# Optimization experiments

Hardware: AMD Instinct MI355X
Metric: run time of the kernel (lower is better)

Reference implementation:

```python
import jax, jax.numpy as jnp
import numpy as np

E, T, D_IN, D_HID, D_OUT = 8, 2048, 1024, 4096, 1024
INTER = 2 * D_HID  # gated (SwiGLU) -> weight1 produces [gate, val]


def setup_inputs() -> dict:
    key = jax.random.key(0)
    k_x, k_w1, k_w2 = jax.random.split(key, 3)
    # kaiming_uniform-ish scale for weights
    x = jax.random.normal(k_x, (E, T, D_IN), dtype=jnp.float32)
    w1 = jax.random.normal(k_w1, (E, D_IN, INTER), dtype=jnp.float32) * (1.0 / np.sqrt(D_IN))
    w2 = jax.random.normal(k_w2, (E, D_HID, D_OUT), dtype=jnp.float32) * (1.0 / np.sqrt(D_HID))
    return {"x": x, "weight1": w1, "weight2": w2}


def reference(x, weight1, weight2):
    # h: [E, T, 2*D_HID] grouped GEMM over experts
    h = jnp.einsum("etd,edi->eti", x, weight1)
    gate, val = jnp.split(h, 2, axis=-1)
    h = jax.nn.silu(gate) * val  # SwiGLU; dropout is identity in eval / p=0
    out = jnp.einsum("eth,eho->eto", h, weight2)  # [E, T, D_OUT]
    return out
```

## Files before the change

### kernel.cpp

```cpp
#include <hip/hip_runtime.h>


#define E_    8
#define T_    2048
#define DIN   1024
#define DHID  4096
#define DOUT  1024
#define INTER 8192

#define NB_W1   16384
#define NB_CONV 2048
#define NB_W2   8192

typedef _Float16 f16;
typedef _Float16 f16x8 __attribute__((ext_vector_type(8)));
typedef float    f32x4 __attribute__((ext_vector_type(4)));

typedef const __attribute__((address_space(1))) void gvoid_t;
typedef __attribute__((address_space(3))) void lvoid_t;

__device__ __forceinline__ void gload_lds16(const void* g, void* l) {
  __builtin_amdgcn_global_load_lds((gvoid_t*)g, (lvoid_t*)l, 16, 0, 0);
}

__device__ __forceinline__ void conv_body(
    const float* __restrict__ src, f16* __restrict__ dst, int n8,
    int bid, int nblk) {
  int i = bid * 256 + threadIdx.x;
  int stride = nblk * 256;
  for (; i < n8; i += stride) {
    const float4* s = (const float4*)(src + (size_t)i * 8);
    float4 a0 = s[0], a1 = s[1];
    f16x8 v;
    v[0] = (f16)a0.x; v[1] = (f16)a0.y; v[2] = (f16)a0.z; v[3] = (f16)a0.w;
    v[4] = (f16)a1.x; v[5] = (f16)a1.y; v[6] = (f16)a1.z; v[7] = (f16)a1.w;
    *(f16x8*)(dst + (size_t)i * 8) = v;
  }
}

template <typename TileT>
__device__ __forceinline__ void xpose64_body(
    const float* __restrict__ src, f16* __restrict__ dst,
    int R, int C, int tC, int bid, TileT& tile) {
  int perE = (R >> 6) * tC;
  int e = bid / perE;
  int rem = bid - e * perE;
  int rt = rem / tC;
  int ct = rem - rt * tC;
  int r0 = rt << 6, c0 = ct << 6;
  int t = threadIdx.x;
  int lr  = t >> 2;
  int lc4 = (t & 3) * 16;
  const float* s = src + (size_t)e * R * C + (size_t)(r0 + lr) * C + c0 + lc4;
#pragma unroll
  for (int i = 0; i < 4; ++i) {
    float4 v = *(const float4*)(s + i * 4);
    tile[lr][lc4 + i * 4 + 0] = (f16)v.x;
    tile[lr][lc4 + i * 4 + 1] = (f16)v.y;
    tile[lr][lc4 + i * 4 + 2] = (f16)v.z;
    tile[lr][lc4 + i * 4 + 3] = (f16)v.w;
  }
  __syncthreads();
  f16* d = dst + (size_t)e * C * R + (size_t)(c0 + lr) * R + r0 + lc4;
  f16x8 o0, o1;
#pragma unroll
  for (int j = 0; j < 8; ++j) o0[j] = tile[lc4 + j][lr];
#pragma unroll
  for (int j = 0; j < 8; ++j) o1[j] = tile[lc4 + 8 + j][lr];
  *(f16x8*)(d)     = o0;
  *(f16x8*)(d + 8) = o1;
}

__global__ __launch_bounds__(256) void prep_all(
    const float* __restrict__ x,  f16* __restrict__ xh,
    const float* __restrict__ w1, f16* __restrict__ w1t,
    const float* __restrict__ w2, f16* __restrict__ w2t) {
  __shared__ f16 tile[64][72];
  int bid = blockIdx.x;
  if (bid < NB_W1) {
    xpose64_body(w1, w1t, DIN, INTER, INTER / 64, bid, tile);
  } else if (bid < NB_W1 + NB_CONV) {
    conv_body(x, xh, E_ * T_ * DIN / 8, bid - NB_W1, NB_CONV);
  } else {
    xpose64_body(w2, w2t, DHID, DOUT, DOUT / 64, bid - (NB_W1 + NB_CONV), tile);
  }
}

__global__ __launch_bounds__(256) void conv_f32_f16(
    const float* __restrict__ src, f16* __restrict__ dst, int n8) {
  conv_body(src, dst, n8, blockIdx.x, gridDim.x);
}

__global__ __launch_bounds__(256) void xpose64_f32_f16(
    const float* __restrict__ src, f16* __restrict__ dst,
    int R, int C, int tC) {
  __shared__ f16 tile[64][72];
  xpose64_body(src, dst, R, C, tC, blockIdx.x, tile);
}

__global__ __launch_bounds__(512, 2) void gemm1_swiglu_xh(
    const f16* __restrict__ xh,
    const f16* __restrict__ w1t,
    f16* __restrict__ hact) {
  __shared__ __align__(1024) f16 As[128][64];
  __shared__ __align__(1024) f16 Bg[128][64];
  __shared__ __align__(1024) f16 Bv[128][64];

  int bid = blockIdx.x;
  int e   = bid >> 9;
  int rem = bid & 511;
  int mt  = rem >> 5;
  int nt  = rem & 31;
  int m0 = mt * 128, n0 = nt * 128;

  const f16* xe = xh  + ((size_t)e * T_ + m0) * DIN;
  const f16* wg = w1t + ((size_t)e * INTER + n0) * DIN;
  const f16* wv = w1t + ((size_t)e * INTER + DHID + n0) * DIN;

  int tid  = threadIdx.x;
  int lane = tid & 63;
  int wid  = tid >> 6;

  int srow8 = lane >> 3;
  int scol  = ((lane & 7) ^ srow8) * 8;

  auto stA = [&](int kt, int i) {
    int ci = wid + 8 * i;
    gload_lds16(xe + (size_t)(ci * 8 + srow8) * DIN + kt * 64 + scol,
                (char*)&As[0][0] + ci * 1024);
  };
  auto stG = [&](int kt, int i) {
    int ci = wid + 8 * i;
    gload_lds16(wg + (size_t)(ci * 8 + srow8) * DIN + kt * 64 + scol,
                (char*)&Bg[0][0] + ci * 1024);
  };
  auto stV = [&](int kt, int i) {
    int ci = wid + 8 * i;
    gload_lds16(wv + (size_t)(ci * 8 + srow8) * DIN + kt * 64 + scol,
                (char*)&Bv[0][0] + ci * 1024);
  };

  int wm  = wid >> 2;
  int wn  = wid & 3;
  int lr  = lane & 15;
  int l16 = lane >> 4;

  f32x4 accG[4][2], accV[4][2];
#pragma unroll
  for (int m = 0; m < 4; ++m)
#pragma unroll
    for (int n = 0; n < 2; ++n) {
      accG[m][n] = f32x4{0.f, 0.f, 0.f, 0.f};
      accV[m][n] = f32x4{0.f, 0.f, 0.f, 0.f};
    }

  for (int kt = 0; kt < DIN / 64; ++kt) {
    __syncthreads();
    stA(kt, 0); stA(kt, 1);
    stG(kt, 0); stG(kt, 1);
    stV(kt, 0); stV(kt, 1);
    __syncthreads();

    f16x8 af[4][2], bg[2][2], bv[2][2];
#pragma unroll
    for (int m = 0; m < 4; ++m)
#pragma unroll
      for (int kk = 0; kk < 2; ++kk) {
        int row_ = wm * 64 + m * 16 + lr;
        af[m][kk] = *(const f16x8*)((const char*)&As[0][0] + row_ * 128 +
                                    (((kk * 4 + l16) ^ (lr & 7)) << 4));
      }
#pragma unroll
    for (int n = 0; n < 2; ++n)
#pragma unroll
      for (int kk = 0; kk < 2; ++kk) {
        int row_ = wn * 32 + n * 16 + lr;
        bg[n][kk] = *(const f16x8*)((const char*)&Bg[0][0] + row_ * 128 +
                                    (((kk * 4 + l16) ^ (lr & 7)) << 4));
        bv[n][kk] = *(const f16x8*)((const char*)&Bv[0][0] + row_ * 128 +
                                    (((kk * 4 + l16) ^ (lr & 7)) << 4));
      }
#pragma unroll
    for (int m = 0; m < 4; ++m)
#pragma unroll
      for (int n = 0; n < 2; ++n)
#pragma unroll
        for (int kk = 0; kk < 2; ++kk) {
          accG[m][n] = __builtin_amdgcn_mfma_f32_16x16x32_f16(af[m][kk], bg[n][kk], accG[m][n], 0, 0, 0);
          accV[m][n] = __builtin_amdgcn_mfma_f32_16x16x32_f16(af[m][kk], bv[n][kk], accV[m][n], 0, 0, 0);
        }
  }

  f16* he = hact + (size_t)e * T_ * DHID;
  int rbase = m0 + wm * 64 + l16 * 4;
  int cbase = n0 + wn * 32 + lr;
#pragma unroll
  for (int m = 0; m < 4; ++m)
#pragma unroll
    for (int n = 0; n < 2; ++n)
#pragma unroll
      for (int j = 0; j < 4; ++j) {
        int row = rbase + m * 16 + j;
        int col = cbase + n * 16;
        float g = accG[m][n][j];
        float v = accV[m][n][j];
        float s = g / (1.0f + __expf(-g));
        he[(size_t)row * DHID + col] = (f16)(s * v);
      }
}

__global__ __launch_bounds__(512, 2) void gemm1_swiglu_rs(
    const float* __restrict__ x,
    const f16* __restrict__ w1t,
    f16* __restrict__ hact) {
  __shared__ f16 As[128][36];
  __shared__ f16 Bg[128][32];
  __shared__ f16 Bv[128][32];

  int bid = blockIdx.x;
  int e   = bid >> 9;
  int rem = bid & 511;
  int mt  = rem >> 5;
  int nt  = rem & 31;
  int m0 = mt * 128, n0 = nt * 128;

  const float* xe = x   + ((size_t)e * T_ + m0) * DIN;
  const f16*   wg = w1t + ((size_t)e * INTER + n0) * DIN;
  const f16*   wv = w1t + ((size_t)e * INTER + DHID + n0) * DIN;

  int tid  = threadIdx.x;
  int lane = tid & 63;
  int wid  = tid >> 6;

  int arow = tid >> 2;
  int acol = (tid & 3) * 8;
  int brow = wid * 16 + (lane >> 2);
  int bcol = (lane & 3) * 8;
  f16* lG = &Bg[wid * 16][0];
  f16* lV = &Bv[wid * 16][0];

  int wm = wid >> 2;
  int wn = wid & 3;
  int lr = lane & 15;
  int lk = (lane >> 4) * 8;

  f32x4 accG[4][2], accV[4][2];
#pragma unroll
  for (int m = 0; m < 4; ++m)
#pragma unroll
    for (int n = 0; n < 2; ++n) {
      accG[m][n] = f32x4{0.f, 0.f, 0.f, 0.f};
      accV[m][n] = f32x4{0.f, 0.f, 0.f, 0.f};
    }

  for (int k = 0; k < DIN; k += 32) {
    __syncthreads();
    gload_lds16(wg + (size_t)brow * DIN + k + bcol, lG);
    gload_lds16(wv + (size_t)brow * DIN + k + bcol, lV);
    {
      const float* sa = xe + (size_t)arow * DIN + k + acol;
      float4 a0 = ((const float4*)sa)[0];
      float4 a1 = ((const float4*)sa)[1];
      f16x8 v;
      v[0] = (f16)a0.x; v[1] = (f16)a0.y; v[2] = (f16)a0.z; v[3] = (f16)a0.w;
      v[4] = (f16)a1.x; v[5] = (f16)a1.y; v[6] = (f16)a1.z; v[7] = (f16)a1.w;
      *(f16x8*)&As[arow][acol] = v;
    }
    __syncthreads();

    f16x8 af[4], bg[2], bv[2];
#pragma unroll
    for (int m = 0; m < 4; ++m)
      af[m] = *(const f16x8*)&As[wm * 64 + m * 16 + lr][lk];
#pragma unroll
    for (int n = 0; n < 2; ++n) {
      bg[n] = *(const f16x8*)&Bg[wn * 32 + n * 16 + lr][lk];
      bv[n] = *(const f16x8*)&Bv[wn * 32 + n * 16 + lr][lk];
    }
#pragma unroll
    for (int m = 0; m < 4; ++m)
#pragma unroll
      for (int n = 0; n < 2; ++n) {
        accG[m][n] = __builtin_amdgcn_mfma_f32_16x16x32_f16(af[m], bg[n], accG[m][n], 0, 0, 0);
        accV[m][n] = __builtin_amdgcn_mfma_f32_16x16x32_f16(af[m], bv[n], accV[m][n], 0, 0, 0);
      }
  }

  f16* he = hact + (size_t)e * T_ * DHID;
  int rbase = m0 + wm * 64 + (lane >> 4) * 4;
  int cbase = n0 + wn * 32 + lr;
#pragma unroll
  for (int m = 0; m < 4; ++m)
#pragma unroll
    for (int n = 0; n < 2; ++n)
#pragma unroll
      for (int j = 0; j < 4; ++j) {
        int row = rbase + m * 16 + j;
        int col = cbase + n * 16;
        float g = accG[m][n][j];
        float v = accV[m][n][j];
        float s = g / (1.0f + __expf(-g));
        he[(size_t)row * DHID + col] = (f16)(s * v);
      }
}

__global__ __launch_bounds__(512, 2) void gemm2_8ph(
    const f16* __restrict__ hact,
    const f16* __restrict__ w2t,
    float* __restrict__ out) {
  __shared__ __align__(1024) f16 As[2][256][64];
  __shared__ __align__(1024) f16 Bs[2][256][64];

  int bid = blockIdx.x;
  int e   = bid >> 5;
  int rem = bid & 31;
  int mt  = rem >> 2;
  int nt  = rem & 3;
  int m0 = mt * 256, n0 = nt * 256;

  const f16* ha = hact + ((size_t)e * T_ + m0) * DHID;
  const f16* wb = w2t  + ((size_t)e * DOUT + n0) * DHID;

  int tid  = threadIdx.x;
  int lane = tid & 63;
  int wid  = tid >> 6;
  int wm   = wid >> 2;
  int wn   = wid & 3;
  int lr   = lane & 15;
  int l16  = lane >> 4;

  int srow = lane >> 3;
  int scol = ((lane & 7) ^ srow) * 8;

  auto stA = [&](int buf, int kt, int i) {
    int ci = wid + 8 * i;
    gload_lds16(ha + (size_t)(ci * 8 + srow) * DHID + kt * 64 + scol,
                (char*)&As[buf][0][0] + ci * 1024);
  };
  auto stB = [&](int buf, int kt, int i) {
    int ci = wid + 8 * i;
    gload_lds16(wb + (size_t)(ci * 8 + srow) * DHID + kt * 64 + scol,
                (char*)&Bs[buf][0][0] + ci * 1024);
  };

  f32x4 acc[8][4];
#pragma unroll
  for (int m = 0; m < 8; ++m)
#pragma unroll
    for (int n = 0; n < 4; ++n) acc[m][n] = f32x4{0.f, 0.f, 0.f, 0.f};

  f16x8 af[4][2], bf0[2][2], bf1[2][2];

#define READ_A2(b, MH)                                                       \
  _Pragma("unroll") for (int m = 0; m < 4; ++m)                              \
  _Pragma("unroll") for (int kk = 0; kk < 2; ++kk) {                         \
    int row_ = wm * 128 + (MH) * 64 + m * 16 + lr;                           \
    af[m][kk] = *(const f16x8*)((const char*)&As[b][0][0] + row_ * 128 +     \
                                (((kk * 4 + l16) ^ (lr & 7)) << 4));         \
  }
#define READ_B2(b, NH, DST)                                                  \
  _Pragma("unroll") for (int n = 0; n < 2; ++n)                              \
  _Pragma("unroll") for (int kk = 0; kk < 2; ++kk) {                         \
    int row_ = wn * 64 + (NH) * 32 + n * 16 + lr;                            \
    DST[n][kk] = *(const f16x8*)((const char*)&Bs[b][0][0] + row_ * 128 +    \
                                 (((kk * 4 + l16) ^ (lr & 7)) << 4));        \
  }
#define MFMA16Q(MH, NH, BB)                                                  \
  __builtin_amdgcn_s_setprio(1);                                            \
  _Pragma("unroll") for (int m = 0; m < 4; ++m)                              \
  _Pragma("unroll") for (int n = 0; n < 2; ++n)                              \
  _Pragma("unroll") for (int kk = 0; kk < 2; ++kk)                          \
    acc[(MH) * 4 + m][(NH) * 2 + n] = __builtin_amdgcn_mfma_f32_16x16x32_f16(\
        af[m][kk], BB[n][kk], acc[(MH) * 4 + m][(NH) * 2 + n], 0, 0, 0);     \
  __builtin_amdgcn_s_setprio(0);
#define BAR() __builtin_amdgcn_s_barrier()
#define LGKM0() asm volatile("s_waitcnt lgkmcnt(0)" ::: "memory")
#define VM6() asm volatile("s_waitcnt vmcnt(6)" ::: "memory")

  stA(0, 0, 0); stA(0, 0, 1); stA(0, 0, 2); stA(0, 0, 3);
  stB(0, 0, 0); stB(0, 0, 1); stB(0, 0, 2); stB(0, 0, 3);
  stB(1, 1, 0); stB(1, 1, 1); stB(1, 1, 2); stB(1, 1, 3);
  stA(1, 1, 0); stA(1, 1, 1);
  VM6();
  BAR();

  for (int it = 0; it < 32; ++it) {
    int tb = 2 * it + 1;
    int pa = (2 * it + 2) & 63;
    int pb = (2 * it + 3) & 63;

    READ_A2(0, 0); READ_B2(0, 0, bf0);
    stA(1, tb, 2); stA(1, tb, 3);
    BAR(); LGKM0();
    MFMA16Q(0, 0, bf0);
    BAR();

    READ_B2(0, 1, bf1);
    BAR(); LGKM0();
    MFMA16Q(0, 1, bf1);
    BAR();

    READ_A2(0, 1);
    stB(0, pa, 0); stB(0, pa, 1);
    BAR(); LGKM0();
    MFMA16Q(1, 0, bf0);
    BAR();

    stB(0, pa, 2); stB(0, pa, 3);
    stA(0, pa, 0); stA(0, pa, 1);
    BAR();
    MFMA16Q(1, 1, bf1);
    VM6();
    BAR();

    READ_A2(1, 0); READ_B2(1, 0, bf0);
    stA(0, pa, 2); stA(0, pa, 3);
    BAR(); LGKM0();
    MFMA16Q(0, 0, bf0);
    BAR();

    READ_B2(1, 1, bf1);
    BAR(); LGKM0();
    MFMA16Q(0, 1, bf1);
    BAR();

    READ_A2(1, 1);
    stB(1, pb, 0); stB(1, pb, 1);
    BAR(); LGKM0();
    MFMA16Q(1, 0, bf0);
    BAR();

    stB(1, pb, 2); stB(1, pb, 3);
    stA(1, pb, 0); stA(1, pb, 1);
    BAR();
    MFMA16Q(1, 1, bf1);
    VM6();
    BAR();
  }

#undef READ_A2
#undef READ_B2
#undef MFMA16Q
#undef BAR
#undef LGKM0
#undef VM6

  float* oe = out + (size_t)e * T_ * DOUT;
  int rbase = m0 + wm * 128 + l16 * 4;
  int cbase = n0 + wn * 64 + lr;
#pragma unroll
  for (int m = 0; m < 8; ++m)
#pragma unroll
    for (int n = 0; n < 4; ++n)
#pragma unroll
      for (int j = 0; j < 4; ++j) {
        int row = rbase + m * 16 + j;
        int col = cbase + n * 16;
        oe[(size_t)row * DOUT + col] = acc[m][n][j];
      }
}

extern "C" void kernel_launch(void* const* d_in, const int* in_sizes, int n_in,
                              void* d_out, int out_size, void* d_ws, size_t ws_size,
                              hipStream_t stream) {
  const float* x  = (const float*)d_in[0];
  const float* w1 = (const float*)d_in[1];
  const float* w2 = (const float*)d_in[2];
  float* out = (float*)d_out;

  const size_t HACT_B = (size_t)E_ * T_ * DHID * 2;
  const size_t W1T_B  = (size_t)E_ * INTER * DIN * 2;
  const size_t W2T_B  = (size_t)E_ * DOUT * DHID * 2;
  const size_t XH_B   = (size_t)E_ * T_ * DIN * 2;

  f16* hact = (f16*)d_ws;
  f16* w1t  = (f16*)((char*)d_ws + HACT_B);

  if (ws_size >= HACT_B + W1T_B + W2T_B + XH_B) {
    f16* w2t = (f16*)((char*)d_ws + HACT_B + W1T_B);
    f16* xxh = (f16*)((char*)d_ws + HACT_B + W1T_B + W2T_B);
    prep_all<<<NB_W1 + NB_CONV + NB_W2, 256, 0, stream>>>(
        x, xxh, w1, w1t, w2, w2t);
    gemm1_swiglu_xh<<<E_ * 16 * 32, 512, 0, stream>>>(xxh, w1t, hact);
    gemm2_8ph<<<E_ * 8 * 4, 512, 0, stream>>>(hact, w2t, out);
  } else if (ws_size >= HACT_B + W1T_B + XH_B) {
    f16* xxh = (f16*)((char*)d_ws + HACT_B + W1T_B);
    xpose64_f32_f16<<<E_ * (DIN / 64) * (INTER / 64), 256, 0, stream>>>(
        w1, w1t, DIN, INTER, INTER / 64);
    conv_f32_f16<<<2048, 256, 0, stream>>>(x, xxh, E_ * T_ * DIN / 8);
    gemm1_swiglu_xh<<<E_ * 16 * 32, 512, 0, stream>>>(xxh, w1t, hact);
    xpose64_f32_f16<<<E_ * (DHID / 64) * (DOUT / 64), 256, 0, stream>>>(
        w2, w1t, DHID, DOUT, DOUT / 64);
    gemm2_8ph<<<E_ * 8 * 4, 512, 0, stream>>>(hact, w1t, out);
  } else {
    xpose64_f32_f16<<<E_ * (DIN / 64) * (INTER / 64), 256, 0, stream>>>(
        w1, w1t, DIN, INTER, INTER / 64);
    gemm1_swiglu_rs<<<E_ * 16 * 32, 512, 0, stream>>>(x, w1t, hact);
    xpose64_f32_f16<<<E_ * (DHID / 64) * (DOUT / 64), 256, 0, stream>>>(
        w2, w1t, DHID, DOUT, DOUT / 64);
    gemm2_8ph<<<E_ * 8 * 4, 512, 0, stream>>>(hact, w1t, out);
  }
}
```

Measured before the change: 567.7 us.

## Fold W2 transpose into GEMM1 launch to overlap with matmul

```diff
diff --git a/kernel.cpp b/kernel.cpp
--- a/kernel.cpp
+++ b/kernel.cpp
@@ -10,7 +10,8 @@
 
 #define NB_W1   16384
 #define NB_CONV 2048
-#define NB_W2   8192
+#define NB_G1   4096
+#define NB_X2   4096
 
 typedef _Float16 f16;
 typedef _Float16 f16x8 __attribute__((ext_vector_type(8)));
@@ -38,17 +39,15 @@
   }
 }
 
-template <typename TileT>
-__device__ __forceinline__ void xpose64_body(
+__device__ __forceinline__ void xpose64_tile(
     const float* __restrict__ src, f16* __restrict__ dst,
-    int R, int C, int tC, int bid, TileT& tile) {
+    int R, int C, int tC, int tileIdx, f16 (*tile)[72], int t) {
   int perE = (R >> 6) * tC;
-  int e = bid / perE;
-  int rem = bid - e * perE;
+  int e = tileIdx / perE;
+  int rem = tileIdx - e * perE;
   int rt = rem / tC;
   int ct = rem - rt * tC;
   int r0 = rt << 6, c0 = ct << 6;
-  int t = threadIdx.x;
   int lr  = t >> 2;
   int lc4 = (t & 3) * 16;
   const float* s = src + (size_t)e * R * C + (size_t)(r0 + lr) * C + c0 + lc4;
@@ -71,18 +70,15 @@
   *(f16x8*)(d + 8) = o1;
 }
 
-__global__ __launch_bounds__(256) void prep_all(
+__global__ __launch_bounds__(256) void prep_w1_conv(
     const float* __restrict__ x,  f16* __restrict__ xh,
-    const float* __restrict__ w1, f16* __restrict__ w1t,
-    const float* __restrict__ w2, f16* __restrict__ w2t) {
+    const float* __restrict__ w1, f16* __restrict__ w1t) {
   __shared__ f16 tile[64][72];
   int bid = blockIdx.x;
   if (bid < NB_W1) {
-    xpose64_body(w1, w1t, DIN, INTER, INTER / 64, bid, tile);
-  } else if (bid < NB_W1 + NB_CONV) {
+    xpose64_tile(w1, w1t, DIN, INTER, INTER / 64, bid, tile, threadIdx.x);
+  } else {
     conv_body(x, xh, E_ * T_ * DIN / 8, bid - NB_W1, NB_CONV);
-  } else {
-    xpose64_body(w2, w2t, DHID, DOUT, DOUT / 64, bid - (NB_W1 + NB_CONV), tile);
   }
 }
 
@@ -95,7 +91,129 @@
     const float* __restrict__ src, f16* __restrict__ dst,
     int R, int C, int tC) {
   __shared__ f16 tile[64][72];
-  xpose64_body(src, dst, R, C, tC, blockIdx.x, tile);
+  xpose64_tile(src, dst, R, C, tC, blockIdx.x, tile, threadIdx.x);
+}
+
+__global__ __launch_bounds__(512, 2) void gemm1_swiglu_w2x(
+    const f16* __restrict__ xh,
+    const f16* __restrict__ w1t,
+    f16* __restrict__ hact,
+    const float* __restrict__ w2,
+    f16* __restrict__ w2t) {
+  __shared__ __align__(1024) f16 As[128][64];
+  __shared__ __align__(1024) f16 Bg[128][64];
+  __shared__ __align__(1024) f16 Bv[128][64];
+
+  int bid = blockIdx.x;
+  if (bid >= NB_G1) {
+    int half = threadIdx.x >> 8;
+    int t    = threadIdx.x & 255;
+    int tileIdx = (bid - NB_G1) * 2 + half;
+    f16 (*tile)[72] = (f16(*)[72])((char*)&As[0][0] + half * 9216);
+    xpose64_tile(w2, w2t, DHID, DOUT, DOUT / 64, tileIdx, tile, t);
+    return;
+  }
+
+  int e   = bid >> 9;
+  int rem = bid & 511;
+  int mt  = rem >> 5;
+  int nt  = rem & 31;
+  int m0 = mt * 128, n0 = nt * 128;
+
+  const f16* xe = xh  + ((size_t)e * T_ + m0) * DIN;
+  const f16* wg = w1t + ((size_t)e * INTER + n0) * DIN;
+  const f16* wv = w1t + ((size_t)e * INTER + DHID + n0) * DIN;
+
+  int tid  = threadIdx.x;
+  int lane = tid & 63;
+  int wid  = tid >> 6;
+
+  int srow8 = lane >> 3;
+  int scol  = ((lane & 7) ^ srow8) * 8;
+
+  auto stA = [&](int kt, int i) {
+    int ci = wid + 8 * i;
+    gload_lds16(xe + (size_t)(ci * 8 + srow8) * DIN + kt * 64 + scol,
+                (char*)&As[0][0] + ci * 1024);
+  };
+  auto stG = [&](int kt, int i) {
+    int ci = wid + 8 * i;
+    gload_lds16(wg + (size_t)(ci * 8 + srow8) * DIN + kt * 64 + scol,
+                (char*)&Bg[0][0] + ci * 1024);
+  };
+  auto stV = [&](int kt, int i) {
+    int ci = wid + 8 * i;
+    gload_lds16(wv + (size_t)(ci * 8 + srow8) * DIN + kt * 64 + scol,
+                (char*)&Bv[0][0] + ci * 1024);
+  };
+
+  int wm  = wid >> 2;
+  int wn  = wid & 3;
+  int lr  = lane & 15;
+  int l16 = lane >> 4;
+
+  f32x4 accG[4][2], accV[4][2];
+#pragma unroll
+  for (int m = 0; m < 4; ++m)
+#pragma unroll
+    for (int n = 0; n < 2; ++n) {
+      accG[m][n] = f32x4{0.f, 0.f, 0.f, 0.f};
+      accV[m][n] = f32x4{0.f, 0.f, 0.f, 0.f};
+    }
+
+  for (int kt = 0; kt < DIN / 64; ++kt) {
+    __syncthreads();
+    stA(kt, 0); stA(kt, 1);
+    stG(kt, 0); stG(kt, 1);
+    stV(kt, 0); stV(kt, 1);
+    __syncthreads();
+
+    f16x8 af[4][2], bg[2][2], bv[2][2];
+#pragma unroll
+    for (int m = 0; m < 4; ++m)
+#pragma unroll
+      for (int kk = 0; kk < 2; ++kk) {
+        int row_ = wm * 64 + m * 16 + lr;
+        af[m][kk] = *(const f16x8*)((const char*)&As[0][0] + row_ * 128 +
+                                    (((kk * 4 + l16) ^ (lr & 7)) << 4));
+      }
+#pragma unroll
+    for (int n = 0; n < 2; ++n)
+#pragma unroll
+      for (int kk = 0; kk < 2; ++kk) {
+        int row_ = wn * 32 + n * 16 + lr;
+        bg[n][kk] = *(const f16x8*)((const char*)&Bg[0][0] + row_ * 128 +
+                                    (((kk * 4 + l16) ^ (lr & 7)) << 4));
+        bv[n][kk] = *(const f16x8*)((const char*)&Bv[0][0] + row_ * 128 +
+                                    (((kk * 4 + l16) ^ (lr & 7)) << 4));
+      }
+#pragma unroll
+    for (int m = 0; m < 4; ++m)
+#pragma unroll
+      for (int n = 0; n < 2; ++n)
+#pragma unroll
+        for (int kk = 0; kk < 2; ++kk) {
+          accG[m][n] = __builtin_amdgcn_mfma_f32_16x16x32_f16(af[m][kk], bg[n][kk], accG[m][n], 0, 0, 0);
+          accV[m][n] = __builtin_amdgcn_mfma_f32_16x16x32_f16(af[m][kk], bv[n][kk], accV[m][n], 0, 0, 0);
+        }
+  }
+
+  f16* he = hact + (size_t)e * T_ * DHID;
+  int rbase = m0 + wm * 64 + l16 * 4;
+  int cbase = n0 + wn * 32 + lr;
+#pragma unroll
+  for (int m = 0; m < 4; ++m)
+#pragma unroll
+    for (int n = 0; n < 2; ++n)
+#pragma unroll
+      for (int j = 0; j < 4; ++j) {
+        int row = rbase + m * 16 + j;
+        int col = cbase + n * 16;
+        float g = accG[m][n][j];
+        float v = accV[m][n][j];
+        float s = g / (1.0f + __expf(-g));
+        he[(size_t)row * DHID + col] = (f16)(s * v);
+      }
 }
 
 __global__ __launch_bounds__(512, 2) void gemm1_swiglu_xh(
@@ -479,9 +597,9 @@
   if (ws_size >= HACT_B + W1T_B + W2T_B + XH_B) {
     f16* w2t = (f16*)((char*)d_ws + HACT_B + W1T_B);
     f16* xxh = (f16*)((char*)d_ws + HACT_B + W1T_B + W2T_B);
-    prep_all<<<NB_W1 + NB_CONV + NB_W2, 256, 0, stream>>>(
-        x, xxh, w1, w1t, w2, w2t);
-    gemm1_swiglu_xh<<<E_ * 16 * 32, 512, 0, stream>>>(xxh, w1t, hact);
+    prep_w1_conv<<<NB_W1 + NB_CONV, 256, 0, stream>>>(x, xxh, w1, w1t);
+    gemm1_swiglu_w2x<<<NB_G1 + NB_X2, 512, 0, stream>>>(
+        xxh, w1t, hact, w2, w2t);
     gemm2_8ph<<<E_ * 8 * 4, 512, 0, stream>>>(hact, w2t, out);
   } else if (ws_size >= HACT_B + W1T_B + XH_B) {
     f16* xxh = (f16*)((char*)d_ws + HACT_B + W1T_B);
```

Result: faster. 556.1 us, median of 2 (-2.0%).
